# Performance work log

Measured on AMD Instinct MI355X. Metric: run time of the kernel, lower is better.

## Reference

```python
import jax, jax.numpy as jnp
import numpy as np

N_NODES = 50000
N_EDGES = 1200000
N_OD = 10000
D_NODE = 16
D_EDGE = 8
HID = 64
N_LAYERS = 3
K_MIN = 1.0
K_MAX = 50.0


def setup_inputs() -> dict:
    key = jax.random.key(0)
    ks = jax.random.split(key, 24)
    s = 0.05
    inp = {
        "node_features": jax.random.normal(ks[0], (N_NODES, D_NODE), jnp.float32),
        "edge_index": jax.random.randint(ks[1], (2, N_EDGES), 0, N_NODES, jnp.int32),
        "edge_features": jax.random.normal(ks[2], (N_EDGES, D_EDGE), jnp.float32),
        "od_pairs": jax.random.randint(ks[3], (2, N_OD), 0, N_NODES, jnp.int32),
        "traffic_stats": jax.random.normal(ks[4], (4,), jnp.float32),
        # projections
        "Wn": jax.random.normal(ks[5], (D_NODE, HID), jnp.float32) * s,
        "bn": jnp.zeros((HID,), jnp.float32),
        "We": jax.random.normal(ks[6], (D_EDGE, HID), jnp.float32) * s,
        "be": jnp.zeros((HID,), jnp.float32),
        # stacked GNN layer weights: message MLP on [h_src, e], update MLP on [h, agg]
        "Wm": jax.random.normal(ks[7], (N_LAYERS, 2 * HID, HID), jnp.float32) * s,
        "bm": jnp.zeros((N_LAYERS, HID), jnp.float32),
        "Wu": jax.random.normal(ks[8], (N_LAYERS, 2 * HID, HID), jnp.float32) * s,
        "bu": jnp.zeros((N_LAYERS, HID), jnp.float32),
        # per-flow score MLP on [h_src, h_dst]
        "Ws1": jax.random.normal(ks[9], (2 * HID, HID), jnp.float32) * s,
        "bs1": jnp.zeros((HID,), jnp.float32),
        "Ws2": jax.random.normal(ks[10], (HID, 1), jnp.float32) * s,
        "bs2": jnp.zeros((1,), jnp.float32),
        # DynamicKHead: Linear(HID+4,32) -> ReLU -> Linear(32,16) -> ReLU -> Linear(16,1)
        "Wk1": jax.random.normal(ks[11], (HID + 4, 32), jnp.float32) * s,
        "bk1": jnp.zeros((32,), jnp.float32),
        "Wk2": jax.random.normal(ks[12], (32, 16), jnp.float32) * s,
        "bk2": jnp.zeros((16,), jnp.float32),
        "Wk3": jax.random.normal(ks[13], (16, 1), jnp.float32) * s,
        "bk3": jnp.zeros((1,), jnp.float32),
    }
    return inp


def _forward(node_features, edge_features, traffic_stats,
             Wn, bn, We, be, Wm, bm, Wu, bu,
             Ws1, bs1, Ws2, bs2, Wk1, bk1, Wk2, bk2, Wk3, bk3,
             edge_index, od_pairs):
    relu = jax.nn.relu
    h = relu(node_features @ Wn + bn)          # [N, HID]
    e = relu(edge_features @ We + be)          # [E, HID]
    src, dst = edge_index[0], edge_index[1]
    for l in range(N_LAYERS):
        # gather-compute-scatter message passing with edge features
        m = relu(jnp.concatenate([h[src], e], axis=-1) @ Wm[l] + bm[l])  # [E, HID]
        agg = jax.ops.segment_sum(m, dst, num_segments=N_NODES)          # [N, HID]
        h = relu(jnp.concatenate([h, agg], axis=-1) @ Wu[l] + bu[l]) + h  # residual
    # per-flow scores from OD endpoint embeddings
    hp = jnp.concatenate([h[od_pairs[0]], h[od_pairs[1]]], axis=-1)      # [P, 2*HID]
    scores = (relu(hp @ Ws1 + bs1) @ Ws2 + bs2).squeeze(-1)              # [P]
    # dynamic-K head (dropout = identity in eval)
    graph_embed = h.mean(axis=0)                                          # [HID]
    x = jnp.concatenate([graph_embed, traffic_stats], axis=-1)
    raw = (relu(relu(x @ Wk1 + bk1) @ Wk2 + bk2) @ Wk3 + bk3).squeeze(-1)
    k_continuous = K_MIN + jax.nn.sigmoid(raw) * (K_MAX - K_MIN)
    return scores, k_continuous


def reference(node_features, edge_index, edge_features, od_pairs, traffic_stats,
              Wn, bn, We, be, Wm, bm, Wu, bu,
              Ws1, bs1, Ws2, bs2, Wk1, bk1, Wk2, bk2, Wk3, bk3):
    return _forward(node_features, edge_features, traffic_stats,
                    Wn, bn, We, be, Wm, bm, Wu, bu,
                    Ws1, bs1, Ws2, bs2, Wk1, bk1, Wk2, bk2, Wk3, bk3,
                    edge_index, od_pairs)
```

## Files before the change

kernel.cpp:

```cpp
#include <hip/hip_runtime.h>
#include <hip/hip_bf16.h>

#define OFF_WN   0
#define OFF_BN   1024
#define OFF_WE   1088
#define OFF_BE   1600
#define OFF_WM   1664
#define OFF_BM   26240
#define OFF_WU   26432
#define OFF_BU   51008
#define OFF_WS1  51200
#define OFF_BS1  59392
#define OFF_WS2  59456
#define OFF_BS2  59520
#define OFF_WK1  59521
#define OFF_BK1  61697
#define OFF_WK2  61729
#define OFF_BK2  62241
#define OFF_WK3  62257
#define OFF_BK3  62273
#define OFF_TS   62274
#define OFF_GSUM 62278
#define OFF_FLAG 62344
#define OFF_BSUM 62400
#define OFF_BOFF 62900
#define OFF_BCUR 63300
#define OFF_H    65536

typedef __attribute__((ext_vector_type(8))) short bfrag;
typedef __attribute__((ext_vector_type(4))) float ffrag;

__device__ __forceinline__ float bf2f(unsigned short u) {
    unsigned int i = ((unsigned int)u) << 16;
    float f;
    __builtin_memcpy(&f, &i, sizeof(f));
    return f;
}
__device__ __forceinline__ float bflo(unsigned int u) {
    unsigned int i = u << 16;
    float f; __builtin_memcpy(&f, &i, sizeof(f)); return f;
}
__device__ __forceinline__ float bfhi(unsigned int u) {
    unsigned int i = u & 0xffff0000u;
    float f; __builtin_memcpy(&f, &i, sizeof(f)); return f;
}
__device__ __forceinline__ unsigned int f2bf_rne(float f) {
    unsigned int u; __builtin_memcpy(&u, &f, 4);
    return (u + 0x7fffu + ((u >> 16) & 1u)) >> 16;
}
__device__ __forceinline__ unsigned int pack2bf(float a, float b) {
    return f2bf_rne(a) | (f2bf_rne(b) << 16);
}
__device__ __forceinline__ unsigned int cvt_pk_bf16(float a, float b) {
    unsigned int r;
    asm("v_cvt_pk_bf16_f32 %0, %1, %2" : "=v"(r) : "v"(a), "v"(b));
    return r;
}

__global__ void detect_dtype_kernel(const unsigned short* __restrict__ nf,
                                    int* __restrict__ flag) {
    int t = threadIdx.x;
    float m = 0.f;
    for (int i = t; i < 1024; i += 64) {
        float v = fabsf(bf2f(nf[i]));
        if (!isnan(v)) m = fmaxf(m, v);
        else m = 1e30f;
    }
    for (int o = 32; o > 0; o >>= 1) m = fmaxf(m, __shfl_down(m, o));
    if (t == 0) flag[0] = (m > 1e6f) ? 1 : 0;
}

struct ConvArgs {
    const void* src[19];
    int off[19];
    int n[19];
};

__global__ __launch_bounds__(256) void convert_all_kernel(
        ConvArgs a, float* __restrict__ ws, const int* __restrict__ flagp) {
    int isf32 = *flagp;
    int ai = blockIdx.y;
    int i  = blockIdx.x * blockDim.x + threadIdx.x;
    if (i < a.n[ai]) {
        float v = isf32 ? ((const float*)a.src[ai])[i]
                        : bf2f(((const unsigned short*)a.src[ai])[i]);
        ws[a.off[ai] + i] = v;
    }
}

__global__ __launch_bounds__(256) void wtrans_prep_kernel(
        const float* __restrict__ ws, short* __restrict__ Wb) {
    int idx = blockIdx.x * 256 + threadIdx.x;
    if (idx < 12288) {
        int l = idx >> 12, rem = idx & 4095, n = rem >> 6, k = rem & 63;
        Wb[idx] = (short)f2bf_rne(ws[OFF_WM + l * 8192 + 4096 + k * 64 + n]);
    } else if (idx < 24576) {
        int j = idx - 12288;
        int l = j >> 12, rem = j & 4095, n = rem >> 6, k = rem & 63;
        Wb[idx] = (short)f2bf_rne(ws[OFF_WM + l * 8192 + k * 64 + n]);
    } else if (idx < 49152) {
        int j = idx - 24576;
        int l = j >> 13, rem = j & 8191, n = rem >> 7, k = rem & 127;
        Wb[idx] = (short)f2bf_rne(ws[OFF_WU + l * 8192 + k * 64 + n]);
    } else if (idx < 51200) {
        int j = idx - 49152;
        int n = j >> 5, k = j & 31;
        Wb[idx] = (k < 8) ? (short)f2bf_rne(ws[OFF_WE + k * 64 + n]) : (short)0;
    } else if (idx < 59392) {
        int j = idx - 51200;
        int n = j >> 7, k = j & 127;
        Wb[idx] = (short)f2bf_rne(ws[OFF_WS1 + k * 64 + n]);
    }
}

__global__ __launch_bounds__(256) void node_proj_kernel(
        const void* __restrict__ nf, const float* __restrict__ ws,
        float* __restrict__ h, int N, const int* __restrict__ flagp) {
    int idx = blockIdx.x * blockDim.x + threadIdx.x;
    if (idx >= N * 64) return;
    int isf32 = *flagp;
    int i = idx >> 6, c = idx & 63;
    const float* Wn = ws + OFF_WN;
    float acc = ws[OFF_BN + c];
    float x[16];
    if (isf32) {
        const float* row = (const float*)nf + (size_t)i * 16;
#pragma unroll
        for (int k = 0; k < 16; ++k) x[k] = row[k];
    } else {
        const unsigned short* row = (const unsigned short*)nf + (size_t)i * 16;
#pragma unroll
        for (int k = 0; k < 16; ++k) x[k] = bf2f(row[k]);
    }
#pragma unroll
    for (int k = 0; k < 16; ++k) acc = fmaf(x[k], Wn[k * 64 + c], acc);
    h[idx] = fmaxf(acc, 0.f);
}

__global__ __launch_bounds__(256) void count_kernel(
        const int* __restrict__ dst, int* __restrict__ deg, int E) {
    int e = blockIdx.x * blockDim.x + threadIdx.x;
    if (e < E) atomicAdd(&deg[dst[e]], 1);
}

__global__ __launch_bounds__(256) void scan_blocks_kernel(
        const int* __restrict__ deg, int* __restrict__ incl,
        int* __restrict__ bsum, int N) {
    int tid = threadIdx.x;
    int gid = blockIdx.x * 256 + tid;
    int v = (gid < N) ? deg[gid] : 0;
    int lane = tid & 63, w = tid >> 6;
    int x = v;
#pragma unroll
    for (int o = 1; o < 64; o <<= 1) {
        int y = __shfl_up(x, o);
        if (lane >= o) x += y;
    }
    __shared__ int wsum[4];
    __shared__ int woff[4];
    if (lane == 63) wsum[w] = x;
    __syncthreads();
    if (tid == 0) {
        int a = 0;
#pragma unroll
        for (int i = 0; i < 4; ++i) { woff[i] = a; a += wsum[i]; }
    }
    __syncthreads();
    x += woff[w];
    if (gid < N) incl[gid] = x;
    if (tid == 255) bsum[blockIdx.x] = x;
}

__global__ __launch_bounds__(256) void scan_bsum_kernel(
        const int* __restrict__ bsum, int* __restrict__ boff, int nb) {
    __shared__ int sh[256];
    int tid = threadIdx.x;
    int carry = 0;
    for (int base = 0; base < nb; base += 256) {
        int v = (base + tid < nb) ? bsum[base + tid] : 0;
        sh[tid] = v;
        __syncthreads();
        for (int o = 1; o < 256; o <<= 1) {
            int t = (tid >= o) ? sh[tid - o] : 0;
            __syncthreads();
            sh[tid] += t;
            __syncthreads();
        }
        if (base + tid < nb) boff[base + tid] = carry + sh[tid] - v;
        __syncthreads();
        carry += sh[255];
        __syncthreads();
    }
}

__global__ __launch_bounds__(256) void scan_finalize_kernel(
        const int* __restrict__ deg, const int* __restrict__ incl,
        const int* __restrict__ boff, int* __restrict__ out,
        int* __restrict__ cursor, int N, int tailval) {
    int gid = blockIdx.x * 256 + threadIdx.x;
    if (gid < N) {
        int ex = boff[blockIdx.x] + incl[gid] - deg[gid];
        out[gid] = ex;
        cursor[gid] = ex;
    }
    if (gid == 0) out[N] = tailval;
}


__global__ __launch_bounds__(256) void fill_passA(
        const int* __restrict__ src, const int* __restrict__ dst,
        const void* __restrict__ ef, const int* __restrict__ off,
        int* __restrict__ bcur, float* __restrict__ interm, int E, int N,
        const int* __restrict__ flagp) {
    __shared__ int hist[256];
    __shared__ int gbase[256];
    const int tid = threadIdx.x;
    const int base = blockIdx.x * 4096;
    const int nbk = (N + 255) >> 8;
    hist[tid] = 0;
    __syncthreads();
    int dd[16], lr[16];
#pragma unroll
    for (int j = 0; j < 16; ++j) {
        int e = base + j * 256 + tid;
        if (e < E) {
            int d = dst[e];
            dd[j] = d;
            lr[j] = atomicAdd(&hist[d >> 8], 1);
        } else dd[j] = -1;
    }
    __syncthreads();
    if (tid < nbk && hist[tid] > 0) {
        int g = atomicAdd(&bcur[tid], hist[tid]);
        gbase[tid] = off[tid << 8] + g;
    }
    __syncthreads();
    int isf32 = *flagp;
#pragma unroll
    for (int j = 0; j < 16; ++j) {
        int e = base + j * 256 + tid;
        if (e >= E) continue;
        unsigned p01, p23, p45, p67;
        if (isf32) {
            const float4* p = (const float4*)ef + (size_t)e * 2;
            float4 a = p[0], b = p[1];
            p01 = pack2bf(a.x, a.y); p23 = pack2bf(a.z, a.w);
            p45 = pack2bf(b.x, b.y); p67 = pack2bf(b.z, b.w);
        } else {
            uint4 r = ((const uint4*)ef)[e];
            p01 = r.x; p23 = r.y; p45 = r.z; p67 = r.w;
        }
        int pos = gbase[dd[j] >> 8] + lr[j];
        float* o = interm + (size_t)pos * 6;
        *(uint2*)o       = make_uint2((unsigned)src[e], (unsigned)dd[j]);
        *(uint2*)(o + 2) = make_uint2(p01, p23);
        *(uint2*)(o + 4) = make_uint2(p45, p67);
    }
}

__global__ __launch_bounds__(256) void fill_passB(
        const float* __restrict__ interm, const int* __restrict__ off,
        float* __restrict__ rec, int N) {
    __shared__ int cur[256];
    const int b = blockIdx.x;
    const int beg = b << 8;
    const int end = (beg + 256 < N) ? beg + 256 : N;
    const int span = end - beg;
    const int tid = threadIdx.x;
    if (tid < span) cur[tid] = off[beg + tid];
    __syncthreads();
    const int k0 = off[beg];
    const int k1 = off[end];
    for (int i = k0 + tid; i < k1; i += 256) {
        const float* ip = interm + (size_t)i * 6;
        uint2 a  = *(const uint2*)ip;
        uint2 bq = *(const uint2*)(ip + 2);
        uint2 c  = *(const uint2*)(ip + 4);
        int slot = atomicAdd(&cur[(int)a.y - beg], 1);
        float* o = rec + (size_t)slot * 6;
        *(uint2*)o       = a;
        *(uint2*)(o + 2) = bq;
        *(uint2*)(o + 4) = c;
    }
}

__global__ __launch_bounds__(256) void fill_fallback(
        const int* __restrict__ src, const int* __restrict__ dst,
        int* __restrict__ cursor, int* __restrict__ eid,
        int* __restrict__ srcs, int E) {
    int e = blockIdx.x * blockDim.x + threadIdx.x;
    if (e >= E) return;
    int pos = atomicAdd(&cursor[dst[e]], 1);
    eid[pos] = e;
    srcs[pos] = src[e];
}

__global__ __launch_bounds__(256) void spans_kernel(
        const int* __restrict__ off, int* __restrict__ spans, int N) {
    int i = blockIdx.x * blockDim.x + threadIdx.x;
    if (i >= N) return;
    int k0 = off[i], k1 = off[i + 1];
    spans[i] = (k1 > k0) ? (((k1 - 1) >> 6) - (k0 >> 6) + 1) : 0;
}

__global__ __launch_bounds__(256) void nodeA_mfma_kernel(
        const short* __restrict__ W1T, const float* __restrict__ bm,
        const float* __restrict__ h, float* __restrict__ A, int N) {
    __shared__ short lds_w[64 * 72];
    __shared__ short lds_x[4][64 * 72];
    const int tid = threadIdx.x, wid = tid >> 6, lane = tid & 63;
    const int r = lane & 15, q = lane >> 4;
    const int nb0 = blockIdx.x * 256 + wid * 64;

#pragma unroll
    for (int j = 0; j < 2; ++j) {
        int f8 = (tid * 2 + j) * 8;
        int row = f8 >> 6, k = f8 & 63;
        *(uint4*)&lds_w[row * 72 + k] = ((const uint4*)W1T)[tid * 2 + j];
    }
    short* xt = &lds_x[wid][0];
#pragma unroll 1
    for (int it = 0; it < 16; ++it) {
        int f4 = it * 64 + lane;
        int node = f4 >> 4, c4 = f4 & 15;
        int gn = nb0 + node; if (gn >= N) gn = N - 1;
        float4 v = ((const float4*)h)[(size_t)gn * 16 + c4];
        *(uint2*)&xt[node * 72 + c4 * 4] =
            make_uint2(pack2bf(v.x, v.y), pack2bf(v.z, v.w));
    }
    __syncthreads();

    bfrag bg[4][2];
#pragma unroll
    for (int ni = 0; ni < 4; ++ni)
#pragma unroll
        for (int ki = 0; ki < 2; ++ki)
            bg[ni][ki] = *(const bfrag*)&lds_w[(ni * 16 + r) * 72 + ki * 32 + q * 8];
    float buv[4];
#pragma unroll
    for (int ni = 0; ni < 4; ++ni) buv[ni] = bm[ni * 16 + r];

    ffrag C[4][4];
#pragma unroll
    for (int mi = 0; mi < 4; ++mi) {
        bfrag af[2];
#pragma unroll
        for (int ki = 0; ki < 2; ++ki)
            af[ki] = *(const bfrag*)&xt[(mi * 16 + r) * 72 + ki * 32 + q * 8];
#pragma unroll
        for (int ni = 0; ni < 4; ++ni) {
            ffrag c = {buv[ni], buv[ni], buv[ni], buv[ni]};
            c = __builtin_amdgcn_mfma_f32_16x16x32_bf16(af[0], bg[ni][0], c, 0, 0, 0);
            c = __builtin_amdgcn_mfma_f32_16x16x32_bf16(af[1], bg[ni][1], c, 0, 0, 0);
            C[mi][ni] = c;
        }
    }
#pragma unroll
    for (int mi = 0; mi < 4; ++mi)
#pragma unroll
        for (int rr = 0; rr < 4; ++rr) {
            int gn = nb0 + mi * 16 + q * 4 + rr;
            if (gn < N) {
#pragma unroll
                for (int ni = 0; ni < 4; ++ni)
                    A[(size_t)gn * 64 + ni * 16 + r] = C[mi][ni][rr];
            }
        }
}

__global__ __launch_bounds__(256, 4) void msg_mfma_red(
        const short* __restrict__ WeT, const float* __restrict__ be,
        const short* __restrict__ WbT, const float* __restrict__ rec,
        const float* __restrict__ A, float* __restrict__ pbuf,
        const int* __restrict__ off, const int* __restrict__ pstart, int E) {
    __shared__ short lds_ev[4][64 * 72];
    __shared__ int   lds_src[4][64];
    const int tid = threadIdx.x;
    const int wid = tid >> 6, lane = tid & 63;
    const int w = blockIdx.x * 4 + wid;
    if (w * 64 >= E) return;
    const int slot = w * 64 + lane;
    const int slotc = (slot < E) ? slot : (E - 1);

    const float* rbase = rec + (size_t)slotc * 6;
    uint2 u0 = *(const uint2*)rbase;
    uint2 u1 = *(const uint2*)(rbase + 2);
    uint2 u2 = *(const uint2*)(rbase + 4);
    int s  = (int)u0.x;
    int di = (int)u0.y;
    int pstv = pstart[di];
    int offv = off[di];
    lds_src[wid][lane] = s;

    short* evb = &lds_ev[wid][0];
    short* evrow = evb + lane * 72;
    *(uint4*)(evrow) = make_uint4(u1.x, u1.y, u2.x, u2.y);
    uint4 z4 = make_uint4(0u, 0u, 0u, 0u);
    *(uint4*)(evrow + 8)  = z4;
    *(uint4*)(evrow + 16) = z4;
    *(uint4*)(evrow + 24) = z4;

    const int r = lane & 15, q = lane >> 4;

    bfrag afe[4];
#pragma unroll
    for (int mi = 0; mi < 4; ++mi)
        afe[mi] = *(const bfrag*)(evb + (mi * 16 + r) * 72 + q * 8);

#pragma unroll
    for (int ni = 0; ni < 4; ++ni) {
        bfrag bge = *(const bfrag*)(WeT + (ni * 16 + r) * 32 + q * 8);
        float4 b4 = *(const float4*)(be + ni * 16 + q * 4);
#pragma unroll
        for (int mi = 0; mi < 4; ++mi) {
            ffrag c = {b4.x, b4.y, b4.z, b4.w};
            c = __builtin_amdgcn_mfma_f32_16x16x32_bf16(bge, afe[mi], c, 0, 0, 0);
            unsigned lo = cvt_pk_bf16(fmaxf(c[0], 0.f), fmaxf(c[1], 0.f));
            unsigned hi = cvt_pk_bf16(fmaxf(c[2], 0.f), fmaxf(c[3], 0.f));
            *(uint2*)(evb + (mi * 16 + r) * 72 + ni * 16 + q * 4) =
                make_uint2(lo, hi);
        }
    }

    bfrag af[4][2];
#pragma unroll
    for (int mi = 0; mi < 4; ++mi)
#pragma unroll
        for (int ki = 0; ki < 2; ++ki)
            af[mi][ki] = *(const bfrag*)(evb + (mi * 16 + r) * 72 + ki * 32 + q * 8);

    const float* ap[4][4];
#pragma unroll
    for (int mi = 0; mi < 4; ++mi) {
        int4 sr = *(const int4*)&lds_src[wid][mi * 16 + q * 4];
        ap[mi][0] = A + (size_t)sr.x * 64 + r;
        ap[mi][1] = A + (size_t)sr.y * 64 + r;
        ap[mi][2] = A + (size_t)sr.z * 64 + r;
        ap[mi][3] = A + (size_t)sr.w * 64 + r;
    }

#pragma unroll
    for (int ni = 0; ni < 4; ++ni) {
        bfrag bg0 = *(const bfrag*)(WbT + (ni * 16 + r) * 64 + q * 8);
        bfrag bg1 = *(const bfrag*)(WbT + (ni * 16 + r) * 64 + 32 + q * 8);
        ffrag C[4];
#pragma unroll
        for (int mi = 0; mi < 4; ++mi) {
            C[mi][0] = ap[mi][0][ni * 16];
            C[mi][1] = ap[mi][1][ni * 16];
            C[mi][2] = ap[mi][2][ni * 16];
            C[mi][3] = ap[mi][3][ni * 16];
        }
#pragma unroll
        for (int mi = 0; mi < 4; ++mi) {
            C[mi] = __builtin_amdgcn_mfma_f32_16x16x32_bf16(af[mi][0], bg0, C[mi], 0, 0, 0);
            C[mi] = __builtin_amdgcn_mfma_f32_16x16x32_bf16(af[mi][1], bg1, C[mi], 0, 0, 0);
        }
#pragma unroll
        for (int mi = 0; mi < 4; ++mi) {
            unsigned lo = cvt_pk_bf16(fmaxf(C[mi][0], 0.f), fmaxf(C[mi][1], 0.f));
            unsigned hi = cvt_pk_bf16(fmaxf(C[mi][2], 0.f), fmaxf(C[mi][3], 0.f));
            *(uint2*)(evb + (ni * 16 + r) * 72 + mi * 16 + q * 4) =
                make_uint2(lo, hi);
        }
    }

    int kmax = E - w * 64; if (kmax > 64) kmax = 64;
    if (kmax < 64) {
        for (int k = kmax; k < 64; ++k) evb[lane * 72 + k] = 0;
    }
    int prevd = __shfl_up(di, 1);
    unsigned long long sm = __ballot(lane != 0 && di != prevd);
    int curp = __shfl(pstv, 0) + (w - (__shfl(offv, 0) >> 6));
    float acc = 0.f;
#pragma unroll
    for (int g = 0; g < 8; ++g) {
        uint4 v = *(const uint4*)(evb + lane * 72 + g * 8);
        float f0 = bflo(v.x), f1 = bfhi(v.x), f2 = bflo(v.y), f3 = bfhi(v.y);
        float f4 = bflo(v.z), f5 = bfhi(v.z), f6 = bflo(v.w), f7 = bfhi(v.w);
        unsigned gm = (unsigned)(sm >> (g * 8)) & 0xffu;
        if (gm == 0) {
            acc += (((f0 + f1) + (f2 + f3)) + ((f4 + f5) + (f6 + f7)));
        } else {
            float fv[8] = {f0, f1, f2, f3, f4, f5, f6, f7};
#pragma unroll
            for (int j = 0; j < 8; ++j) {
                if (gm & (1u << j)) {
                    pbuf[(size_t)curp * 64 + lane] = acc;
                    acc = 0.f;
                    curp = __shfl(pstv, g * 8 + j);
                }
                acc += fv[j];
            }
        }
    }
    pbuf[(size_t)curp * 64 + lane] = acc;
}

__global__ __launch_bounds__(256) void fixup_kernel(
        const float* __restrict__ pbuf, const int* __restrict__ off,
        const int* __restrict__ pstart, float* __restrict__ agg, int N) {
    int tid = blockIdx.x * blockDim.x + threadIdx.x;
    int i = tid >> 2, q = tid & 3;
    if (i >= N) return;
    int k0 = off[i], k1 = off[i + 1];
    float acc[16];
#pragma unroll
    for (int c = 0; c < 16; ++c) acc[c] = 0.f;
    if (k1 > k0) {
        int nsp = ((k1 - 1) >> 6) - (k0 >> 6) + 1;
        int p = pstart[i];
        for (int j = 0; j < nsp; ++j) {
            const float4* pr = (const float4*)(pbuf + (size_t)(p + j) * 64 + q * 16);
#pragma unroll
            for (int c = 0; c < 4; ++c) {
                float4 v = pr[c];
                acc[4 * c] += v.x; acc[4 * c + 1] += v.y;
                acc[4 * c + 2] += v.z; acc[4 * c + 3] += v.w;
            }
        }
    }
    float4* o4 = (float4*)(agg + (size_t)i * 64 + q * 16);
#pragma unroll
    for (int c = 0; c < 4; ++c)
        o4[c] = make_float4(acc[4 * c], acc[4 * c + 1], acc[4 * c + 2], acc[4 * c + 3]);
}

__global__ __launch_bounds__(128) void update_mfma_kernel(
        const short* __restrict__ WuT, const float* __restrict__ bu,
        float* __restrict__ h, const float* __restrict__ agg, int N) {
    __shared__ short lds_w[64 * 136];
    __shared__ short lds_x[2][64 * 136];
    const int tid = threadIdx.x, wid = tid >> 6, lane = tid & 63;
    const int r = lane & 15, q = lane >> 4;
    const int nb0 = blockIdx.x * 128 + wid * 64;
#pragma unroll
    for (int j = 0; j < 8; ++j) {
        int f8 = (tid * 8 + j) * 8;
        int row = f8 >> 7, k = f8 & 127;
        *(uint4*)&lds_w[row * 136 + k] = ((const uint4*)WuT)[tid * 8 + j];
    }
    short* xt = &lds_x[wid][0];
#pragma unroll 1
    for (int it = 0; it < 32; ++it) {
        int f4 = it * 64 + lane;
        int node = f4 >> 5, c4 = f4 & 31;
        int gn = nb0 + node; if (gn >= N) gn = N - 1;
        const float4* src = (c4 < 16)
            ? ((const float4*)h + (size_t)gn * 16 + c4)
            : ((const float4*)agg + (size_t)gn * 16 + (c4 - 16));
        float4 v = *src;
        *(uint2*)&xt[node * 136 + c4 * 4] =
            make_uint2(pack2bf(v.x, v.y), pack2bf(v.z, v.w));
    }
    __syncthreads();
    bfrag bg[4][4];
#pragma unroll
    for (int ni = 0; ni < 4; ++ni)
#pragma unroll
        for (int ki = 0; ki < 4; ++ki)
            bg[ni][ki] = *(const bfrag*)&lds_w[(ni * 16 + r) * 136 + ki * 32 + q * 8];
    float buv[4];
#pragma unroll
    for (int ni = 0; ni < 4; ++ni) buv[ni] = bu[ni * 16 + r];
    ffrag C[4][4];
#pragma unroll
    for (int mi = 0; mi < 4; ++mi) {
        bfrag af[4];
#pragma unroll
        for (int ki = 0; ki < 4; ++ki)
            af[ki] = *(const bfrag*)&xt[(mi * 16 + r) * 136 + ki * 32 + q * 8];
#pragma unroll
        for (int ni = 0; ni < 4; ++ni) {
            ffrag c = {buv[ni], buv[ni], buv[ni], buv[ni]};
#pragma unroll
            for (int ki = 0; ki < 4; ++ki)
                c = __builtin_amdgcn_mfma_f32_16x16x32_bf16(af[ki], bg[ni][ki], c, 0, 0, 0);
            C[mi][ni] = c;
        }
    }
#pragma unroll
    for (int mi = 0; mi < 4; ++mi)
#pragma unroll
        for (int rr = 0; rr < 4; ++rr) {
            int nl = mi * 16 + q * 4 + rr;
            int gn = nb0 + nl;
            if (gn < N) {
#pragma unroll
                for (int ni = 0; ni < 4; ++ni) {
                    float hold = bf2f((unsigned short)xt[nl * 136 + ni * 16 + r]);
                    h[(size_t)gn * 64 + ni * 16 + r] =
                        fmaxf(C[mi][ni][rr], 0.f) + hold;
                }
            }
        }
}

__global__ __launch_bounds__(256) void gather_msg_fallback(
        const float* __restrict__ Wm2, const float* __restrict__ We,
        const float* __restrict__ be, const void* __restrict__ ef,
        const int* __restrict__ srcs, const int* __restrict__ eid,
        const int* __restrict__ off, const float* __restrict__ A,
        float* __restrict__ agg, int N, const int* __restrict__ flagp) {
    int i = blockIdx.x * blockDim.x + threadIdx.x;
    if (i >= N) return;
    int isf32 = *flagp;
    int k0 = off[i], k1 = off[i + 1];
    float acc[64];
#pragma unroll
    for (int c = 0; c < 64; ++c) acc[c] = 0.f;
    for (int k = k0; k < k1; ++k) {
        int s = srcs[k];
        int e = eid[k];
        const float4* a4 = (const float4*)(A + (size_t)s * 64);
        float t[64];
#pragma unroll
        for (int c = 0; c < 16; ++c) {
            float4 v = a4[c];
            t[4 * c] = v.x; t[4 * c + 1] = v.y; t[4 * c + 2] = v.z; t[4 * c + 3] = v.w;
        }
        float efv[8];
        if (isf32) {
            const float4* e4 = (const float4*)ef + (size_t)e * 2;
            float4 ra = e4[0], rb = e4[1];
            efv[0]=ra.x; efv[1]=ra.y; efv[2]=ra.z; efv[3]=ra.w;
            efv[4]=rb.x; efv[5]=rb.y; efv[6]=rb.z; efv[7]=rb.w;
        } else {
            uint4 rr = ((const uint4*)ef)[e];
            efv[0]=bflo(rr.x); efv[1]=bfhi(rr.x); efv[2]=bflo(rr.y); efv[3]=bfhi(rr.y);
            efv[4]=bflo(rr.z); efv[5]=bfhi(rr.z); efv[6]=bflo(rr.w); efv[7]=bfhi(rr.w);
        }
#pragma unroll 1
        for (int d0 = 0; d0 < 64; d0 += 8) {
            float ev[8];
#pragma unroll
            for (int dd = 0; dd < 8; ++dd) {
                float a = be[d0 + dd];
#pragma unroll
                for (int kk = 0; kk < 8; ++kk) a = fmaf(efv[kk], We[kk * 64 + d0 + dd], a);
                ev[dd] = fmaxf(a, 0.f);
            }
#pragma unroll
            for (int dd = 0; dd < 8; ++dd) {
                const float* w = Wm2 + (d0 + dd) * 64;
#pragma unroll
                for (int c = 0; c < 64; ++c) t[c] = fmaf(ev[dd], w[c], t[c]);
            }
        }
#pragma unroll
        for (int c = 0; c < 64; ++c) acc[c] += fmaxf(t[c], 0.f);
    }
    float4* o4 = (float4*)(agg + (size_t)i * 64);
#pragma unroll
    for (int c = 0; c < 16; ++c)
        o4[c] = make_float4(acc[4 * c], acc[4 * c + 1], acc[4 * c + 2], acc[4 * c + 3]);
}

__global__ __launch_bounds__(128) void scores_mfma_kernel(
        const short* __restrict__ Ws1T, const float* __restrict__ bs1,
        const float* __restrict__ Ws2, const float* __restrict__ bs2,
        const int* __restrict__ ods, const int* __restrict__ odd,
        const float* __restrict__ h, void* __restrict__ out, int P,
        const int* __restrict__ flagp) {
    __shared__ short lds_w[64 * 136];
    __shared__ short lds_x[2][64 * 136];
    const int tid = threadIdx.x, wid = tid >> 6, lane = tid & 63;
    const int r = lane & 15, q = lane >> 4;
    const int pb0 = blockIdx.x * 128 + wid * 64;
#pragma unroll
    for (int j = 0; j < 8; ++j) {
        int f8 = (tid * 8 + j) * 8;
        int row = f8 >> 7, k = f8 & 127;
        *(uint4*)&lds_w[row * 136 + k] = ((const uint4*)Ws1T)[tid * 8 + j];
    }
    short* xt = &lds_x[wid][0];
#pragma unroll 1
    for (int it = 0; it < 32; ++it) {
        int f4 = it * 64 + lane;
        int pr = f4 >> 5, c4 = f4 & 31;
        int gp = pb0 + pr; if (gp >= P) gp = P - 1;
        int node = (c4 < 16) ? ods[gp] : odd[gp];
        int cc = (c4 < 16) ? c4 : (c4 - 16);
        float4 v = ((const float4*)h)[(size_t)node * 16 + cc];
        *(uint2*)&xt[pr * 136 + c4 * 4] =
            make_uint2(pack2bf(v.x, v.y), pack2bf(v.z, v.w));
    }
    __syncthreads();

    bfrag bg[4][4];
#pragma unroll
    for (int ni = 0; ni < 4; ++ni)
#pragma unroll
        for (int ki = 0; ki < 4; ++ki)
            bg[ni][ki] = *(const bfrag*)&lds_w[(ni * 16 + r) * 136 + ki * 32 + q * 8];
    float buv[4], w2v[4];
#pragma unroll
    for (int ni = 0; ni < 4; ++ni) { buv[ni] = bs1[ni * 16 + r]; w2v[ni] = Ws2[ni * 16 + r]; }
    int isf32 = *flagp;
    float b2 = bs2[0];

#pragma unroll
    for (int mi = 0; mi < 4; ++mi) {
        bfrag af[4];
#pragma unroll
        for (int ki = 0; ki < 4; ++ki)
            af[ki] = *(const bfrag*)&xt[(mi * 16 + r) * 136 + ki * 32 + q * 8];
        float part[4] = {0.f, 0.f, 0.f, 0.f};
#pragma unroll
        for (int ni = 0; ni < 4; ++ni) {
            ffrag c = {buv[ni], buv[ni], buv[ni], buv[ni]};
#pragma unroll
            for (int ki = 0; ki < 4; ++ki)
                c = __builtin_amdgcn_mfma_f32_16x16x32_bf16(af[ki], bg[ni][ki], c, 0, 0, 0);
#pragma unroll
            for (int rr = 0; rr < 4; ++rr)
                part[rr] = fmaf(fmaxf(c[rr], 0.f), w2v[ni], part[rr]);
        }
#pragma unroll
        for (int rr = 0; rr < 4; ++rr) {
            float v = part[rr];
            v += __shfl_xor(v, 1); v += __shfl_xor(v, 2);
            v += __shfl_xor(v, 4); v += __shfl_xor(v, 8);
            if (r == 0) {
                int p = pb0 + mi * 16 + q * 4 + rr;
                if (p < P) {
                    float score = v + b2;
                    if (isf32) ((float*)out)[p] = score;
                    else ((__hip_bfloat16*)out)[p] = __float2bfloat16(score);
                }
            }
        }
    }
}

__global__ __launch_bounds__(256) void embed_kernel(
        const float* __restrict__ h, float* __restrict__ gsum, int N) {
    __shared__ float red[256];
    int c = threadIdx.x & 63;
    int sub = threadIdx.x >> 6;
    float a = 0.f;
    for (int i = blockIdx.x * 4 + sub; i < N; i += gridDim.x * 4)
        a += h[(size_t)i * 64 + c];
    red[threadIdx.x] = a;
    __syncthreads();
    if (threadIdx.x < 64) {
        float t = red[threadIdx.x] + red[threadIdx.x + 64] +
                  red[threadIdx.x + 128] + red[threadIdx.x + 192];
        unsafeAtomicAdd(&gsum[threadIdx.x], t);
    }
}

__global__ void khead_kernel(const float* __restrict__ ws,
                             void* __restrict__ out, int N, int P,
                             const int* __restrict__ flagp) {
    __shared__ float sh1[32];
    __shared__ float sh2[16];
    int lane = threadIdx.x;
    float invN = 1.f / (float)N;
    float a1 = (lane < 32) ? ws[OFF_BK1 + lane] : 0.f;
#pragma unroll
    for (int i = 0; i < 68; ++i) {
        float xi = (i < 64) ? ws[OFF_GSUM + i] * invN : ws[OFF_TS + i - 64];
        if (lane < 32) a1 = fmaf(xi, ws[OFF_WK1 + i * 32 + lane], a1);
    }
    if (lane < 32) sh1[lane] = fmaxf(a1, 0.f);
    __syncthreads();
    float a2 = (lane < 16) ? ws[OFF_BK2 + lane] : 0.f;
#pragma unroll
    for (int j = 0; j < 32; ++j) {
        if (lane < 16) a2 = fmaf(sh1[j], ws[OFF_WK2 + j * 16 + lane], a2);
    }
    if (lane < 16) sh2[lane] = fmaxf(a2, 0.f);
    __syncthreads();
    if (lane == 0) {
        float raw = ws[OFF_BK3];
#pragma unroll
        for (int k2 = 0; k2 < 16; ++k2) raw = fmaf(sh2[k2], ws[OFF_WK3 + k2], raw);
        float sig = 1.f / (1.f + expf(-raw));
        float k = 1.f + 49.f * sig;
        if (*flagp) ((float*)out)[P] = k;
        else ((__hip_bfloat16*)out)[P] = __float2bfloat16(k);
    }
}

extern "C" void kernel_launch(void* const* d_in, const int* in_sizes, int n_in,
                              void* d_out, int out_size, void* d_ws, size_t ws_size,
                              hipStream_t stream) {
    const void* nf = d_in[0];
    const int*  ei = (const int*)d_in[1];
    const void* ef = d_in[2];
    const int*  od = (const int*)d_in[3];
    float* ws = (float*)d_ws;

    const int N = in_sizes[0] / 16;
    const int E = in_sizes[1] / 2;
    const int P = in_sizes[3] / 2;

    float* h      = ws + OFF_H;
    float* agg    = h + (size_t)N * 64;
    float* A      = agg + (size_t)N * 64;
    int*   deg    = (int*)(A + (size_t)N * 64);
    int*   off    = deg + N;
    int*   cursor = off + N + 1;
    int*   pstart = cursor + N;
    int*   eid    = pstart + N + 1;
    int*   srcs   = eid + E;
    short* WbT    = (short*)(srcs + E);
    short* W1T    = WbT + 12288;
    short* WuT    = WbT + 24576;
    short* WeT    = WbT + 49152;
    short* Ws1T   = WbT + 51200;
    int*   flag   = (int*)(ws + OFF_FLAG);
    int*   bsum   = (int*)(ws + OFF_BSUM);
    int*   boff   = (int*)(ws + OFF_BOFF);
    int*   bcur   = (int*)(ws + OFF_BCUR);

    size_t fsofar = (size_t)OFF_H + 3 * (size_t)N * 64
                  + (size_t)(N + (N + 1) + N + (N + 1) + E + E) + 29696;
    size_t recOff = (fsofar + 7) & ~(size_t)7;
    float* rec = ws + recOff;
    size_t pbufOff = recOff + (size_t)E * 6;
    float* pbuf = ws + pbufOff;
    float* interm = pbuf;
    long pbufRows = (long)N + E / 64 + 128;
    size_t tailFloats = (size_t)pbufRows * 64;
    size_t intermFloats = (size_t)E * 6;
    if (intermFloats > tailFloats) tailFloats = intermFloats;
    size_t needBytes = (pbufOff + tailFloats) * sizeof(float);
    const bool big = (ws_size >= needBytes);

    const int* srcv = ei;
    const int* dstv = ei + E;

    detect_dtype_kernel<<<1, 64, 0, stream>>>((const unsigned short*)nf, flag);

    ConvArgs ca;
    const int srcidx[19] = {5, 6, 7, 8, 9, 10, 11, 12, 13, 14, 15, 16, 17, 18, 19, 20, 21, 22, 4};
    const int wsoff[19]  = {OFF_WN, OFF_BN, OFF_WE, OFF_BE, OFF_WM, OFF_BM, OFF_WU, OFF_BU,
                            OFF_WS1, OFF_BS1, OFF_WS2, OFF_BS2, OFF_WK1, OFF_BK1, OFF_WK2,
                            OFF_BK2, OFF_WK3, OFF_BK3, OFF_TS};
    int maxn = 0;
    for (int i = 0; i < 19; ++i) {
        ca.src[i] = d_in[srcidx[i]];
        ca.off[i] = wsoff[i];
        ca.n[i]   = in_sizes[srcidx[i]];
        if (ca.n[i] > maxn) maxn = ca.n[i];
    }
    dim3 cgrid((maxn + 255) / 256, 19);
    convert_all_kernel<<<cgrid, 256, 0, stream>>>(ca, ws, flag);
    wtrans_prep_kernel<<<232, 256, 0, stream>>>(ws, WbT);

    node_proj_kernel<<<(N * 64 + 255) / 256, 256, 0, stream>>>(nf, ws, h, N, flag);

    hipMemsetAsync(deg, 0, (size_t)N * sizeof(int), stream);
    count_kernel<<<(E + 255) / 256, 256, 0, stream>>>(dstv, deg, E);
    int nb = (N + 255) / 256;
    scan_blocks_kernel<<<nb, 256, 0, stream>>>(deg, cursor, bsum, N);
    scan_bsum_kernel<<<1, 256, 0, stream>>>(bsum, boff, nb);
    scan_finalize_kernel<<<nb, 256, 0, stream>>>(deg, cursor, boff, off, cursor, N, E);
    if (big) {
        hipMemsetAsync(bcur, 0, 256 * sizeof(int), stream);
        fill_passA<<<(E + 4095) / 4096, 256, 0, stream>>>(
            srcv, dstv, ef, off, bcur, interm, E, N, flag);
        fill_passB<<<(N + 255) / 256, 256, 0, stream>>>(interm, off, rec, N);
    } else {
        fill_fallback<<<(E + 255) / 256, 256, 0, stream>>>(
            srcv, dstv, cursor, eid, srcs, E);
    }

    if (big) {
        spans_kernel<<<nb, 256, 0, stream>>>(off, deg, N);
        scan_blocks_kernel<<<nb, 256, 0, stream>>>(deg, cursor, bsum, N);
        scan_bsum_kernel<<<1, 256, 0, stream>>>(bsum, boff, nb);
        scan_finalize_kernel<<<nb, 256, 0, stream>>>(deg, cursor, boff, pstart, cursor, N, 0);
    }

    const int N4 = N * 4;
    const int mblocks = (E + 255) / 256;
    const int ablocks = (N + 255) / 256;
    const int ublocks = (N + 127) / 128;
    for (int l = 0; l < 3; ++l) {
        nodeA_mfma_kernel<<<ablocks, 256, 0, stream>>>(
            W1T + l * 4096, ws + OFF_BM + l * 64, h, A, N);
        if (big) {
            msg_mfma_red<<<mblocks, 256, 0, stream>>>(
                WeT, ws + OFF_BE, WbT + l * 4096, rec, A, pbuf, off, pstart, E);
            fixup_kernel<<<(N4 + 255) / 256, 256, 0, stream>>>(
                pbuf, off, pstart, agg, N);
        } else {
            const float* Wm2 = ws + OFF_WM + l * 8192 + 4096;
            gather_msg_fallback<<<(N + 255) / 256, 256, 0, stream>>>(
                Wm2, ws + OFF_WE, ws + OFF_BE, ef, srcs, eid, off, A, agg, N, flag);
        }
        update_mfma_kernel<<<ublocks, 128, 0, stream>>>(
            WuT + l * 8192, ws + OFF_BU + l * 64, h, agg, N);
    }

    scores_mfma_kernel<<<(P + 127) / 128, 128, 0, stream>>>(
        Ws1T, ws + OFF_BS1, ws + OFF_WS2, ws + OFF_BS2,
        od, od + P, h, d_out, P, flag);

    hipMemsetAsync(ws + OFF_GSUM, 0, 64 * sizeof(float), stream);
    embed_kernel<<<256, 256, 0, stream>>>(h, ws + OFF_GSUM, N);
    khead_kernel<<<1, 64, 0, stream>>>(ws, d_out, N, P, flag);
}
```

Before: 582.9 us.

## Prefetch gathered source rows in registers and widen fill kernels to 1024 threads

The message kernel now broadcasts source indices with wave shuffles instead of staging them in LDS, and gathers the A rows for the next output column block into registers while the current block's MFMAs run, a software-pipelined prefetch. The two CSR fill passes launch 1024-thread blocks that each handle 4 edges per thread instead of 16, for more parallelism per block. This costs extra VGPRs in the message kernel, which may lower occupancy under the 4-blocks launch bound. The histogram guard now uses tid<256 instead of the bucket count, which is only safe if buckets past N stay zero.

```diff
diff --git a/kernel.cpp b/kernel.cpp
--- a/kernel.cpp
+++ b/kernel.cpp
@@ -207,7 +207,7 @@
 }
 
 
-__global__ __launch_bounds__(256) void fill_passA(
+__global__ __launch_bounds__(1024) void fill_passA(
         const int* __restrict__ src, const int* __restrict__ dst,
         const void* __restrict__ ef, const int* __restrict__ off,
         int* __restrict__ bcur, float* __restrict__ interm, int E, int N,
@@ -216,13 +216,12 @@
     __shared__ int gbase[256];
     const int tid = threadIdx.x;
     const int base = blockIdx.x * 4096;
-    const int nbk = (N + 255) >> 8;
-    hist[tid] = 0;
-    __syncthreads();
-    int dd[16], lr[16];
-#pragma unroll
-    for (int j = 0; j < 16; ++j) {
-        int e = base + j * 256 + tid;
+    if (tid < 256) hist[tid] = 0;
+    __syncthreads();
+    int dd[4], lr[4];
+#pragma unroll
+    for (int j = 0; j < 4; ++j) {
+        int e = base + j * 1024 + tid;
         if (e < E) {
             int d = dst[e];
             dd[j] = d;
@@ -230,15 +229,15 @@
         } else dd[j] = -1;
     }
     __syncthreads();
-    if (tid < nbk && hist[tid] > 0) {
+    if (tid < 256 && hist[tid] > 0) {
         int g = atomicAdd(&bcur[tid], hist[tid]);
         gbase[tid] = off[tid << 8] + g;
     }
     __syncthreads();
     int isf32 = *flagp;
 #pragma unroll
-    for (int j = 0; j < 16; ++j) {
-        int e = base + j * 256 + tid;
+    for (int j = 0; j < 4; ++j) {
+        int e = base + j * 1024 + tid;
         if (e >= E) continue;
         unsigned p01, p23, p45, p67;
         if (isf32) {
@@ -258,7 +257,7 @@
     }
 }
 
-__global__ __launch_bounds__(256) void fill_passB(
+__global__ __launch_bounds__(1024) void fill_passB(
         const float* __restrict__ interm, const int* __restrict__ off,
         float* __restrict__ rec, int N) {
     __shared__ int cur[256];
@@ -271,7 +270,7 @@
     __syncthreads();
     const int k0 = off[beg];
     const int k1 = off[end];
-    for (int i = k0 + tid; i < k1; i += 256) {
+    for (int i = k0 + tid; i < k1; i += 1024) {
         const float* ip = interm + (size_t)i * 6;
         uint2 a  = *(const uint2*)ip;
         uint2 bq = *(const uint2*)(ip + 2);
@@ -374,7 +373,6 @@
         const float* __restrict__ A, float* __restrict__ pbuf,
         const int* __restrict__ off, const int* __restrict__ pstart, int E) {
     __shared__ short lds_ev[4][64 * 72];
-    __shared__ int   lds_src[4][64];
     const int tid = threadIdx.x;
     const int wid = tid >> 6, lane = tid & 63;
     const int w = blockIdx.x * 4 + wid;
@@ -390,7 +388,17 @@
     int di = (int)u0.y;
     int pstv = pstart[di];
     int offv = off[di];
-    lds_src[wid][lane] = s;
+
+    const int r = lane & 15, q = lane >> 4;
+
+    int srow[16];
+#pragma unroll
+    for (int k = 0; k < 16; ++k)
+        srow[k] = __shfl(s, (k >> 2) * 16 + q * 4 + (k & 3));
+    float cur[16];
+#pragma unroll
+    for (int k = 0; k < 16; ++k)
+        cur[k] = A[(size_t)srow[k] * 64 + r];
 
     short* evb = &lds_ev[wid][0];
     short* evrow = evb + lane * 72;
@@ -400,8 +408,6 @@
     *(uint4*)(evrow + 16) = z4;
     *(uint4*)(evrow + 24) = z4;
 
-    const int r = lane & 15, q = lane >> 4;
-
     bfrag afe[4];
 #pragma unroll
     for (int mi = 0; mi < 4; ++mi)
@@ -429,27 +435,23 @@
         for (int ki = 0; ki < 2; ++ki)
             af[mi][ki] = *(const bfrag*)(evb + (mi * 16 + r) * 72 + ki * 32 + q * 8);
 
-    const float* ap[4][4];
-#pragma unroll
-    for (int mi = 0; mi < 4; ++mi) {
-        int4 sr = *(const int4*)&lds_src[wid][mi * 16 + q * 4];
-        ap[mi][0] = A + (size_t)sr.x * 64 + r;
-        ap[mi][1] = A + (size_t)sr.y * 64 + r;
-        ap[mi][2] = A + (size_t)sr.z * 64 + r;
-        ap[mi][3] = A + (size_t)sr.w * 64 + r;
-    }
-
 #pragma unroll
     for (int ni = 0; ni < 4; ++ni) {
+        float nxt[16];
+        if (ni < 3) {
+#pragma unroll
+            for (int k = 0; k < 16; ++k)
+                nxt[k] = A[(size_t)srow[k] * 64 + (ni + 1) * 16 + r];
+        }
         bfrag bg0 = *(const bfrag*)(WbT + (ni * 16 + r) * 64 + q * 8);
         bfrag bg1 = *(const bfrag*)(WbT + (ni * 16 + r) * 64 + 32 + q * 8);
         ffrag C[4];
 #pragma unroll
         for (int mi = 0; mi < 4; ++mi) {
-            C[mi][0] = ap[mi][0][ni * 16];
-            C[mi][1] = ap[mi][1][ni * 16];
-            C[mi][2] = ap[mi][2][ni * 16];
-            C[mi][3] = ap[mi][3][ni * 16];
+            C[mi][0] = cur[mi * 4 + 0];
+            C[mi][1] = cur[mi * 4 + 1];
+            C[mi][2] = cur[mi * 4 + 2];
+            C[mi][3] = cur[mi * 4 + 3];
         }
 #pragma unroll
         for (int mi = 0; mi < 4; ++mi) {
@@ -462,6 +464,10 @@
             unsigned hi = cvt_pk_bf16(fmaxf(C[mi][2], 0.f), fmaxf(C[mi][3], 0.f));
             *(uint2*)(evb + (ni * 16 + r) * 72 + mi * 16 + q * 4) =
                 make_uint2(lo, hi);
+        }
+        if (ni < 3) {
+#pragma unroll
+            for (int k = 0; k < 16; ++k) cur[k] = nxt[k];
         }
     }
 
@@ -860,9 +866,9 @@
     scan_finalize_kernel<<<nb, 256, 0, stream>>>(deg, cursor, boff, off, cursor, N, E);
     if (big) {
         hipMemsetAsync(bcur, 0, 256 * sizeof(int), stream);
-        fill_passA<<<(E + 4095) / 4096, 256, 0, stream>>>(
+        fill_passA<<<(E + 4095) / 4096, 1024, 0, stream>>>(
             srcv, dstv, ef, off, bcur, interm, E, N, flag);
-        fill_passB<<<(N + 255) / 256, 256, 0, stream>>>(interm, off, rec, N);
+        fill_passB<<<nb, 1024, 0, stream>>>(interm, off, rec, N);
     } else {
         fill_fallback<<<(E + 255) / 256, 256, 0, stream>>>(
             srcv, dstv, cursor, eid, srcs, E);
```

Measured after the change: 591.0 us. Within noise of the previous version (+1.4%).
